# Kernel optimization log

Measured on AMD Instinct MI355X. Metric: run time of the kernel, lower is better.

## Reference

```python
import jax, jax.numpy as jnp
import numpy as np

ARITY = 2
DEPTH = 11          # full tree: levels 0..DEPTH, leaves at DEPTH
H = 1024
V = 32001           # vocab_size + 1 (null token)


def _preorder_perm(depth, arity):
    """Permutation mapping pre-order position -> BFS (level-concatenated) index."""
    offsets = np.concatenate([[0], np.cumsum(arity ** np.arange(depth + 1))])
    order = []
    def rec(d, p):
        order.append(int(offsets[d] + p))
        if d < depth:
            for c in range(arity):
                rec(d + 1, p * arity + c)
    rec(0, 0)
    return np.asarray(order, dtype=np.int32)

_PERM = _preorder_perm(DEPTH, ARITY)


def setup_inputs() -> dict:
    key = jax.random.key(0)
    ks = jax.random.split(key, 9)
    s = 0.02  # small init scale for numerical sanity
    return {
        "root_hidden": jax.random.normal(ks[0], (H,), jnp.float32),
        "W1v": jax.random.normal(ks[1], (H, 2 * H), jnp.float32) * s,
        "b1v": jax.random.normal(ks[2], (2 * H,), jnp.float32) * s,
        "W2v": jax.random.normal(ks[3], (2 * H, V), jnp.float32) * s,
        "b2v": jax.random.normal(ks[4], (V,), jnp.float32) * s,
        "W1c": jax.random.normal(ks[5], (H, 2 * H), jnp.float32) * s,
        "b1c": jax.random.normal(ks[6], (2 * H,), jnp.float32) * s,
        "W2c": jax.random.normal(ks[7], (2 * H, ARITY * H), jnp.float32) * s,
        "b2c": jax.random.normal(ks[8], (ARITY * H,), jnp.float32) * s,
    }


def _mlp(h, W1, b1, W2, b2):
    # Linear -> Sigmoid -> Linear (matches nn.Sequential in the torch module)
    return jax.nn.sigmoid(h @ W1 + b1) @ W2 + b2


def reference(root_hidden, W1v, b1v, W2v, b2v, W1c, b1c, W2c, b2c):
    # Level-wise vectorized sweep over the full tree (batches all nodes at a depth).
    h = root_hidden[None, :]                  # [1, H]
    prods = []
    for d in range(DEPTH + 1):
        prods.append(_mlp(h, W1v, b1v, W2v, b2v))     # [a^d, V]
        if d < DEPTH:
            # to_children then split into arity children per node
            h = _mlp(h, W1c, b1c, W2c, b2c).reshape(-1, H)  # [a^(d+1), H]
    raw = jnp.concatenate(prods, axis=0)      # BFS order, [N, V]
    raw = raw[_PERM]                          # reorder to pre-order (torch recursion order)
    return jax.nn.log_softmax(raw, axis=1)
```

## Files before the change

kernel.cpp:

```cpp
#include <hip/hip_runtime.h>
#include <hip/hip_bf16.h>

#define DEPTH_T 11
#define HDIM 1024
#define VDIM 32001
#define NNODES 4095
#define LDV 32008

typedef __attribute__((ext_vector_type(8))) short bf16x8;
typedef __attribute__((ext_vector_type(8))) unsigned short ushort8;
typedef __attribute__((ext_vector_type(4))) float floatx4;

__device__ __forceinline__ int preorder_pos(int m) {
    int q = m + 1;
    int d = 31 - __clz(q);
    int pos = 0;
    for (int i = 1; i <= d; ++i) {
        int b = (q >> (d - i)) & 1;
        pos += 1 + b * ((1 << (DEPTH_T - i + 1)) - 1);
    }
    return pos;
}

__device__ __forceinline__ float bf2f(unsigned short u) {
    return __uint_as_float(((unsigned)u) << 16);
}

#define BM 128
#define BN 128
#define BK 32

template<int MODE, bool SWAPG>
__global__ __launch_bounds__(256, 2) void gemm_bt(
    const __hip_bfloat16* __restrict__ A,
    const __hip_bfloat16* __restrict__ Bt,
    const float* __restrict__ bias,
    void* __restrict__ outp,
    int M, int N, int K, int ldout)
{
    __shared__ __align__(16) __hip_bfloat16 As[BM][BK];
    __shared__ __align__(16) __hip_bfloat16 Bs[BN][BK];

    const int tid  = threadIdx.x;
    const int wave = tid >> 6;
    const int lane = tid & 63;
    const int m0 = (SWAPG ? blockIdx.x : blockIdx.y) * BM;
    const int n0 = (SWAPG ? blockIdx.y : blockIdx.x) * BN;
    const int wm = (wave & 1) * 64;
    const int wn = (wave >> 1) * 64;

    floatx4 acc[4][4];
#pragma unroll
    for (int i = 0; i < 4; ++i)
#pragma unroll
        for (int j = 0; j < 4; ++j) acc[i][j] = (floatx4)0.0f;

    const int lrow = lane >> 2;
    const int lcol = (lane & 3) * 8;
    const int fr = lane & 15;
    const int fk = (lane >> 4) * 8;

    for (int k0 = 0; k0 < K; k0 += BK) {
        __syncthreads();
#pragma unroll
        for (int t = 0; t < 2; ++t) {
            const int r = (wave * 2 + t) * 16;
            int gm = m0 + r + lrow; gm = gm < M ? gm : M - 1;
            const __hip_bfloat16* gp = A + (size_t)gm * K + (k0 + lcol);
            __builtin_amdgcn_global_load_lds(
                (const __attribute__((address_space(1))) void*)gp,
                (__attribute__((address_space(3))) void*)(&As[r][0]),
                16, 0, 0);
        }
#pragma unroll
        for (int t = 0; t < 2; ++t) {
            const int r = (wave * 2 + t) * 16;
            int gn = n0 + r + lrow; gn = gn < N ? gn : N - 1;
            const __hip_bfloat16* gp = Bt + (size_t)gn * K + (k0 + lcol);
            __builtin_amdgcn_global_load_lds(
                (const __attribute__((address_space(1))) void*)gp,
                (__attribute__((address_space(3))) void*)(&Bs[r][0]),
                16, 0, 0);
        }
        __syncthreads();

        bf16x8 af[4], bfv[4];
#pragma unroll
        for (int i = 0; i < 4; ++i)
            af[i] = *(const bf16x8*)(&As[wm + i * 16 + fr][fk]);
#pragma unroll
        for (int j = 0; j < 4; ++j)
            bfv[j] = *(const bf16x8*)(&Bs[wn + j * 16 + fr][fk]);
#pragma unroll
        for (int i = 0; i < 4; ++i)
#pragma unroll
            for (int j = 0; j < 4; ++j)
                acc[i][j] = __builtin_amdgcn_mfma_f32_16x16x32_bf16(
                    af[i], bfv[j], acc[i][j], 0, 0, 0);
    }

    const int rq = (lane >> 4) * 4;
    if (MODE >= 2) {
#pragma unroll
        for (int i = 0; i < 4; ++i) {
#pragma unroll
            for (int r = 0; r < 4; ++r) {
                const int gm = m0 + wm + i * 16 + rq + r;
                if (gm >= M) continue;
                const size_t orow = (size_t)preorder_pos(gm) * ldout;
#pragma unroll
                for (int j = 0; j < 4; ++j) {
                    const int gn = n0 + wn + j * 16 + fr;
                    if (gn < N) {
                        float v = acc[i][j][r] + bias[gn];
                        if (MODE == 2) ((float*)outp)[orow + gn] = v;
                        else ((__hip_bfloat16*)outp)[orow + gn] = __float2bfloat16(v);
                    }
                }
            }
        }
    } else {
        __hip_bfloat16* O = (__hip_bfloat16*)outp;
#pragma unroll
        for (int i = 0; i < 4; ++i) {
#pragma unroll
            for (int r = 0; r < 4; ++r) {
                const int gm = m0 + wm + i * 16 + rq + r;
                if (gm >= M) continue;
#pragma unroll
                for (int j = 0; j < 4; ++j) {
                    const int gn = n0 + wn + j * 16 + fr;
                    if (gn < N) {
                        float v = acc[i][j][r] + bias[gn];
                        if (MODE == 0) v = 1.0f / (1.0f + __expf(-v));
                        O[(size_t)gm * ldout + gn] = __float2bfloat16(v);
                    }
                }
            }
        }
    }
}

#define B2M 256
#define B2N 256

template<int MODE>
__global__ __launch_bounds__(512, 2) void gemm256(
    const __hip_bfloat16* __restrict__ A,
    const __hip_bfloat16* __restrict__ Bt,
    const float* __restrict__ bias,
    void* __restrict__ outp,
    int M, int N, int K, int ldout)
{
    __shared__ __align__(16) char smem[131072];

    const int tid  = threadIdx.x;
    const int wave = tid >> 6;
    const int lane = tid & 63;
    const int m0 = blockIdx.x * B2M;
    const int n0 = blockIdx.y * B2N;
    const int wm = (wave >> 2) * 128;
    const int wn = (wave & 3) * 64;
    const int nkt = K >> 6;

    const int s_row = lane >> 3;
    const int s_col = ((lane & 7) ^ s_row) * 8;

    const int fr  = lane & 15;
    const int fkq = lane >> 4;
    const int swz = (fr & 7) << 4;
    const int c0  = (fkq * 16) ^ swz;
    const int c1  = (64 + fkq * 16) ^ swz;
    const int aoff = (wm + fr) * 128;
    const int boff = 32768 + (wn + fr) * 128;

    floatx4 acc[8][4];
#pragma unroll
    for (int i = 0; i < 8; ++i)
#pragma unroll
        for (int j = 0; j < 4; ++j) acc[i][j] = (floatx4)0.0f;

    bf16x8 a0[8], a1[8], b0[4], b1[4];

    auto stage = [&](int bsel, int mat, int h, int kt) {
        const int ktc = kt < nkt ? kt : 0;
        const __hip_bfloat16* gb = mat ? Bt : A;
        const int lim = mat ? N : M;
        const int g0  = mat ? n0 : m0;
#pragma unroll
        for (int inst = 0; inst < 2; ++inst) {
            const int rg = inst * 8 + wave;
            int gr = g0 + h * 128 + rg * 8 + s_row;
            gr = gr < lim ? gr : lim - 1;
            const __hip_bfloat16* gp = gb + (size_t)gr * K + (ktc * 64 + s_col);
            __builtin_amdgcn_global_load_lds(
                (const __attribute__((address_space(1))) void*)gp,
                (__attribute__((address_space(3))) void*)
                    (smem + bsel * 65536 + mat * 32768 + h * 16384 + rg * 1024),
                16, 0, 0);
        }
    };

#define RD_A(dst, bsel, cc) \
    _Pragma("unroll") \
    for (int i = 0; i < 8; ++i) \
        dst[i] = *(const bf16x8*)(smem + (bsel) * 65536 + aoff + i * 2048 + (cc));
#define RD_B(dst, bsel, cc) \
    _Pragma("unroll") \
    for (int j = 0; j < 4; ++j) \
        dst[j] = *(const bf16x8*)(smem + (bsel) * 65536 + boff + j * 2048 + (cc));
#define MM(ib, AA, BB) \
    _Pragma("unroll") \
    for (int i = 0; i < 4; ++i) \
    _Pragma("unroll") \
    for (int j = 0; j < 4; ++j) \
        acc[(ib) + i][j] = __builtin_amdgcn_mfma_f32_16x16x32_bf16( \
            AA[(ib) + i], BB[j], acc[(ib) + i][j], 0, 0, 0);
#define LGKM0  asm volatile("s_waitcnt lgkmcnt(0)" ::: "memory")
#define VM4    asm volatile("s_waitcnt vmcnt(4)" ::: "memory")
#define BAR    __builtin_amdgcn_s_barrier()
#define PRIO1  __builtin_amdgcn_s_setprio(1)
#define PRIO0  __builtin_amdgcn_s_setprio(0)

    stage(0, 0, 0, 0);
    stage(0, 0, 1, 0);
    stage(0, 1, 0, 0);
    stage(0, 1, 1, 0);
    stage(1, 0, 0, 1);
    stage(1, 0, 1, 1);
    VM4;
    BAR;

#pragma unroll 1
    for (int t = 0; t < nkt; t += 2) {
        RD_A(a0, 0, c0); RD_B(b0, 0, c0);
        stage(1, 1, 0, t + 1);
        BAR; LGKM0;
        PRIO1; MM(0, a0, b0); PRIO0;
        BAR;
        RD_A(a1, 0, c1); RD_B(b1, 0, c1);
        stage(1, 1, 1, t + 1);
        BAR; LGKM0;
        PRIO1; MM(4, a0, b0); PRIO0;
        BAR;
        stage(0, 0, 0, t + 2);
        BAR;
        PRIO1; MM(0, a1, b1); PRIO0;
        BAR;
        stage(0, 0, 1, t + 2);
        VM4;
        BAR;
        PRIO1; MM(4, a1, b1); PRIO0;
        BAR;
        RD_A(a0, 1, c0); RD_B(b0, 1, c0);
        stage(0, 1, 0, t + 2);
        BAR; LGKM0;
        PRIO1; MM(0, a0, b0); PRIO0;
        BAR;
        RD_A(a1, 1, c1); RD_B(b1, 1, c1);
        stage(0, 1, 1, t + 2);
        BAR; LGKM0;
        PRIO1; MM(4, a0, b0); PRIO0;
        BAR;
        stage(1, 0, 0, t + 3);
        BAR;
        PRIO1; MM(0, a1, b1); PRIO0;
        BAR;
        stage(1, 0, 1, t + 3);
        VM4;
        BAR;
        PRIO1; MM(4, a1, b1); PRIO0;
        BAR;
    }

#undef RD_A
#undef RD_B
#undef MM
#undef LGKM0
#undef VM4
#undef BAR
#undef PRIO1
#undef PRIO0

    const int rq = (lane >> 4) * 4;
    if (MODE >= 2) {
#pragma unroll
        for (int i = 0; i < 8; ++i) {
#pragma unroll
            for (int r = 0; r < 4; ++r) {
                const int gm = m0 + wm + i * 16 + rq + r;
                if (gm >= M) continue;
                const size_t orow = (size_t)preorder_pos(gm) * ldout;
#pragma unroll
                for (int j = 0; j < 4; ++j) {
                    const int gn = n0 + wn + j * 16 + fr;
                    if (gn < N) {
                        float v = acc[i][j][r] + bias[gn];
                        if (MODE == 2) ((float*)outp)[orow + gn] = v;
                        else ((__hip_bfloat16*)outp)[orow + gn] = __float2bfloat16(v);
                    }
                }
            }
        }
    } else {
        __hip_bfloat16* O = (__hip_bfloat16*)outp;
#pragma unroll
        for (int i = 0; i < 8; ++i) {
#pragma unroll
            for (int r = 0; r < 4; ++r) {
                const int gm = m0 + wm + i * 16 + rq + r;
                if (gm >= M) continue;
#pragma unroll
                for (int j = 0; j < 4; ++j) {
                    const int gn = n0 + wn + j * 16 + fr;
                    if (gn < N) {
                        float v = acc[i][j][r] + bias[gn];
                        if (MODE == 0) v = 1.0f / (1.0f + __expf(-v));
                        O[(size_t)gm * ldout + gn] = __float2bfloat16(v);
                    }
                }
            }
        }
    }
}

template<int MODE>
__global__ __launch_bounds__(256) void gemm_small(
    const __hip_bfloat16* __restrict__ A,
    const __hip_bfloat16* __restrict__ Bt,
    const float* __restrict__ bias,
    __hip_bfloat16* __restrict__ O,
    int M, int N, int K)
{
    const int wave = threadIdx.x >> 6, lane = threadIdx.x & 63;
    const int n0 = blockIdx.x * 64 + wave * 16;
    const int m0 = blockIdx.y * 16;
    const int fr = lane & 15, fk = (lane >> 4) * 8;

    int am = m0 + fr; am = am < M ? am : M - 1;
    const __hip_bfloat16* ap = A + (size_t)am * K + fk;
    const __hip_bfloat16* bp = Bt + (size_t)(n0 + fr) * K + fk;

    floatx4 acc = (floatx4)0.0f;
#pragma unroll 8
    for (int k0 = 0; k0 < K; k0 += 32) {
        bf16x8 av = *(const bf16x8*)(ap + k0);
        bf16x8 bv = *(const bf16x8*)(bp + k0);
        acc = __builtin_amdgcn_mfma_f32_16x16x32_bf16(av, bv, acc, 0, 0, 0);
    }

    const int rq = (lane >> 4) * 4;
    const int gn = n0 + fr;
    const float b = bias[gn];
#pragma unroll
    for (int r = 0; r < 4; ++r) {
        const int gm = m0 + rq + r;
        if (gm >= M) continue;
        float v = acc[r] + b;
        if (MODE == 0) v = 1.0f / (1.0f + __expf(-v));
        O[(size_t)gm * N + gn] = __float2bfloat16(v);
    }
}

__global__ __launch_bounds__(256) void transpose_to_bf16(
    const float* __restrict__ in, __hip_bfloat16* __restrict__ outT, int R, int C)
{
    __shared__ float tile[64][65];
    const int c0 = blockIdx.x * 64, r0 = blockIdx.y * 64;
    const int tx = threadIdx.x & 63, ty = threadIdx.x >> 6;
#pragma unroll
    for (int i = 0; i < 64; i += 4) {
        int r = r0 + ty + i, c = c0 + tx;
        tile[ty + i][tx] = (r < R && c < C) ? in[(size_t)r * C + c] : 0.0f;
    }
    __syncthreads();
#pragma unroll
    for (int i = 0; i < 64; i += 4) {
        int rr = c0 + ty + i, cc = r0 + tx;
        if (rr < C && cc < R) outT[(size_t)rr * R + cc] = __float2bfloat16(tile[tx][ty + i]);
    }
}

__global__ __launch_bounds__(256) void convert_root(
    const float* __restrict__ in, __hip_bfloat16* __restrict__ out)
{
    int i = blockIdx.x * 256 + threadIdx.x;
    if (i < HDIM) out[i] = __float2bfloat16(in[i]);
}

__global__ __launch_bounds__(256) void logsoftmax_bf16(
    const unsigned short* __restrict__ L, float* __restrict__ O)
{
    extern __shared__ char smem[];
    unsigned short* rb = (unsigned short*)smem;
    float* wred = (float*)(smem + 64016);
    const int tid = threadIdx.x, lane = tid & 63, wv = tid >> 6;
    const unsigned short* src = L + (size_t)blockIdx.x * LDV;

    float m = -3.0e38f;
    for (int j = tid * 8; j < 32000; j += 2048) {
        ushort8 u = *(const ushort8*)(src + j);
        *(ushort8*)(rb + j) = u;
#pragma unroll
        for (int t = 0; t < 8; ++t) m = fmaxf(m, bf2f(u[t]));
    }
    if (tid == 0) { unsigned short u = src[32000]; rb[32000] = u; m = fmaxf(m, bf2f(u)); }
#pragma unroll
    for (int off = 32; off; off >>= 1) m = fmaxf(m, __shfl_xor(m, off, 64));
    if (lane == 0) wred[wv] = m;
    __syncthreads();
    const float M4 = fmaxf(fmaxf(wred[0], wred[1]), fmaxf(wred[2], wred[3]));

    float s = 0.0f;
    for (int j = tid * 8; j < 32000; j += 2048) {
        ushort8 u = *(const ushort8*)(rb + j);
#pragma unroll
        for (int t = 0; t < 8; ++t) s += __expf(bf2f(u[t]) - M4);
    }
    if (tid == 0) s += __expf(bf2f(rb[32000]) - M4);
#pragma unroll
    for (int off = 32; off; off >>= 1) s += __shfl_xor(s, off, 64);
    if (lane == 0) wred[4 + wv] = s;
    __syncthreads();
    const float lse = M4 + __logf(wred[4] + wred[5] + wred[6] + wred[7]);

    float* dst = O + (size_t)blockIdx.x * VDIM;
    for (int j = tid * 8; j < 32000; j += 2048) {
        ushort8 u = *(const ushort8*)(rb + j);
#pragma unroll
        for (int t = 0; t < 8; ++t) dst[j + t] = bf2f(u[t]) - lse;
    }
    if (tid == 0) dst[32000] = bf2f(rb[32000]) - lse;
}

__global__ __launch_bounds__(256) void logsoftmax_rows(float* __restrict__ O, int n)
{
    __shared__ float sm[256], ssum[256];
    const int tid = threadIdx.x;
    float* p = O + (size_t)blockIdx.x * n;
    float m = -3.0e38f, s = 0.0f;
    for (int j = tid; j < n; j += 256) {
        float x = p[j];
        float nm = fmaxf(m, x);
        s = s * __expf(m - nm) + __expf(x - nm);
        m = nm;
    }
    sm[tid] = m; ssum[tid] = s;
    __syncthreads();
    for (int off = 128; off > 0; off >>= 1) {
        if (tid < off) {
            float m2 = sm[tid + off], s2 = ssum[tid + off];
            float nm = fmaxf(sm[tid], m2);
            ssum[tid] = ssum[tid] * __expf(sm[tid] - nm) + s2 * __expf(m2 - nm);
            sm[tid] = nm;
        }
        __syncthreads();
    }
    const float lse = sm[0] + __logf(ssum[0]);
    for (int j = tid; j < n; j += 256) p[j] -= lse;
}

extern "C" void kernel_launch(void* const* d_in, const int* in_sizes, int n_in,
                              void* d_out, int out_size, void* d_ws, size_t ws_size,
                              hipStream_t stream)
{
    const float* root = (const float*)d_in[0];
    const float* W1v  = (const float*)d_in[1];
    const float* b1v  = (const float*)d_in[2];
    const float* W2v  = (const float*)d_in[3];
    const float* b2v  = (const float*)d_in[4];
    const float* W1c  = (const float*)d_in[5];
    const float* b1c  = (const float*)d_in[6];
    const float* W2c  = (const float*)d_in[7];
    const float* b2c  = (const float*)d_in[8];

    char* ws = (char*)d_ws;
    __hip_bfloat16* Hall = (__hip_bfloat16*)(ws + 0);
    __hip_bfloat16* X1   = (__hip_bfloat16*)(ws +   8388608ull);
    __hip_bfloat16* Tt   = (__hip_bfloat16*)(ws +  25165824ull);
    __hip_bfloat16* W1vT = (__hip_bfloat16*)(ws +  29360128ull);
    __hip_bfloat16* W1cT = (__hip_bfloat16*)(ws +  33554432ull);
    __hip_bfloat16* W2cT = (__hip_bfloat16*)(ws +  37748736ull);
    __hip_bfloat16* W2vT = (__hip_bfloat16*)(ws +  46137344ull);
    __hip_bfloat16* Lb   = (__hip_bfloat16*)(ws + 177213440ull);
    const bool bf16_logits = ws_size >= 177213440ull + (size_t)NNODES * LDV * 2;

    dim3 blk(256);

    transpose_to_bf16<<<dim3( 32, 16), blk, 0, stream>>>(W1v, W1vT, 1024, 2048);
    transpose_to_bf16<<<dim3(501, 32), blk, 0, stream>>>(W2v, W2vT, 2048, VDIM);
    transpose_to_bf16<<<dim3( 32, 16), blk, 0, stream>>>(W1c, W1cT, 1024, 2048);
    transpose_to_bf16<<<dim3( 32, 32), blk, 0, stream>>>(W2c, W2cT, 2048, 2048);
    convert_root<<<dim3(4), blk, 0, stream>>>(root, Hall);

    for (int d = 0; d < DEPTH_T; ++d) {
        const int Md = 1 << d;
        __hip_bfloat16* Hd = Hall + (size_t)(Md - 1) * HDIM;
        __hip_bfloat16* Hn = Hall + (size_t)((2 << d) - 1) * HDIM;
        if (Md <= 256) {
            dim3 g(32, (Md + 15) / 16);
            gemm_small<0><<<g, blk, 0, stream>>>(Hd, W1cT, b1c, Tt, Md, 2048, 1024);
            gemm_small<1><<<g, blk, 0, stream>>>(Tt, W2cT, b2c, Hn, Md, 2048, 2048);
        } else {
            dim3 g(16, Md / 128);
            gemm_bt<0, false><<<g, blk, 0, stream>>>(Hd, W1cT, b1c, Tt, Md, 2048, 1024, 2048);
            gemm_bt<1, false><<<g, blk, 0, stream>>>(Tt, W2cT, b2c, Hn, Md, 2048, 2048, 2048);
        }
    }

    gemm_bt<0, false><<<dim3(16, 32), blk, 0, stream>>>(Hall, W1vT, b1v, X1, NNODES, 2048, 1024, 2048);
    if (bf16_logits) {
        gemm256<3><<<dim3(16, 126), dim3(512), 0, stream>>>(X1, W2vT, b2v, Lb, NNODES, VDIM, 2048, LDV);
        logsoftmax_bf16<<<dim3(NNODES), blk, 64048, stream>>>((const unsigned short*)Lb, (float*)d_out);
    } else {
        gemm_bt<2, true><<<dim3(32, 251), blk, 0, stream>>>(X1, W2vT, b2v, d_out, NNODES, VDIM, 2048, VDIM);
        logsoftmax_rows<<<dim3(NNODES), blk, 0, stream>>>((float*)d_out, VDIM);
    }
}
```

Baseline: 1.460 ms.

## Restructure 256x256 GEMM main loop into quadrant MFMA phases with XCD-aware block remap

The big vocab GEMM's k-loop is rewritten so LDS fragment reads are split into lo/hi halves of A and B. Each of four MFMA quadrant phases can then start after only partial lgkmcnt waits, with B tiles prefetched one stage earlier and sched_barriers pinning the order. The launch grid becomes 1D, and block ids are remapped so consecutive tiles land on the same XCD, aiming for better L2 reuse on the chiplet GPU. This adds more registers, finely tuned waitcnt counts and extra prologue loads, which risks correctness or stalls if the counts are wrong.

```diff
diff --git a/kernel.cpp b/kernel.cpp
--- a/kernel.cpp
+++ b/kernel.cpp
@@ -157,8 +157,15 @@
     const int tid  = threadIdx.x;
     const int wave = tid >> 6;
     const int lane = tid & 63;
-    const int m0 = blockIdx.x * B2M;
-    const int n0 = blockIdx.y * B2N;
+
+    const int nwx = (M + B2M - 1) / B2M;
+    const int nwy = (N + B2N - 1) / B2N;
+    const int nwg = nwx * nwy;
+    int wg = blockIdx.x;
+    if ((nwg & 7) == 0) wg = (wg & 7) * (nwg >> 3) + (wg >> 3);
+    const int m0 = (wg % nwx) * B2M;
+    const int n0 = (wg / nwx) * B2N;
+
     const int wm = (wave >> 2) * 128;
     const int wn = (wave & 3) * 64;
     const int nkt = K >> 6;
@@ -180,7 +187,7 @@
 #pragma unroll
         for (int j = 0; j < 4; ++j) acc[i][j] = (floatx4)0.0f;
 
-    bf16x8 a0[8], a1[8], b0[4], b1[4];
+    bf16x8 alo[8], ahi[8], blo[4], bhi[4];
 
     auto stage = [&](int bsel, int mat, int h, int kt) {
         const int ktc = kt < nkt ? kt : 0;
@@ -201,23 +208,39 @@
         }
     };
 
-#define RD_A(dst, bsel, cc) \
-    _Pragma("unroll") \
-    for (int i = 0; i < 8; ++i) \
-        dst[i] = *(const bf16x8*)(smem + (bsel) * 65536 + aoff + i * 2048 + (cc));
-#define RD_B(dst, bsel, cc) \
-    _Pragma("unroll") \
-    for (int j = 0; j < 4; ++j) \
-        dst[j] = *(const bf16x8*)(smem + (bsel) * 65536 + boff + j * 2048 + (cc));
-#define MM(ib, AA, BB) \
-    _Pragma("unroll") \
-    for (int i = 0; i < 4; ++i) \
-    _Pragma("unroll") \
-    for (int j = 0; j < 4; ++j) \
-        acc[(ib) + i][j] = __builtin_amdgcn_mfma_f32_16x16x32_bf16( \
-            AA[(ib) + i], BB[j], acc[(ib) + i][j], 0, 0, 0);
-#define LGKM0  asm volatile("s_waitcnt lgkmcnt(0)" ::: "memory")
-#define VM4    asm volatile("s_waitcnt vmcnt(4)" ::: "memory")
+#define RD_ALO(bsel) \
+    _Pragma("unroll") \
+    for (int f = 0; f < 4; ++f) { \
+        alo[f*2+0] = *(const bf16x8*)(smem + (bsel)*65536 + aoff + f*2048 + c0); \
+        alo[f*2+1] = *(const bf16x8*)(smem + (bsel)*65536 + aoff + f*2048 + c1); }
+#define RD_AHI(bsel) \
+    _Pragma("unroll") \
+    for (int f = 0; f < 4; ++f) { \
+        ahi[f*2+0] = *(const bf16x8*)(smem + (bsel)*65536 + aoff + (4+f)*2048 + c0); \
+        ahi[f*2+1] = *(const bf16x8*)(smem + (bsel)*65536 + aoff + (4+f)*2048 + c1); }
+#define RD_BLO(bsel) \
+    _Pragma("unroll") \
+    for (int j = 0; j < 2; ++j) { \
+        blo[j*2+0] = *(const bf16x8*)(smem + (bsel)*65536 + boff + j*2048 + c0); \
+        blo[j*2+1] = *(const bf16x8*)(smem + (bsel)*65536 + boff + j*2048 + c1); }
+#define RD_BHI(bsel) \
+    _Pragma("unroll") \
+    for (int j = 0; j < 2; ++j) { \
+        bhi[j*2+0] = *(const bf16x8*)(smem + (bsel)*65536 + boff + (2+j)*2048 + c0); \
+        bhi[j*2+1] = *(const bf16x8*)(smem + (bsel)*65536 + boff + (2+j)*2048 + c1); }
+#define MM_Q(IB, JB, AA, BB) \
+    _Pragma("unroll") \
+    for (int f = 0; f < 4; ++f) \
+    _Pragma("unroll") \
+    for (int jj = 0; jj < 2; ++jj) \
+    _Pragma("unroll") \
+    for (int ks = 0; ks < 2; ++ks) \
+        acc[(IB)+f][(JB)+jj] = __builtin_amdgcn_mfma_f32_16x16x32_bf16( \
+            AA[f*2+ks], BB[jj*2+ks], acc[(IB)+f][(JB)+jj], 0, 0, 0);
+
+#define VMC(n)  asm volatile("s_waitcnt vmcnt(" #n ")" ::: "memory")
+#define LGKM(n) asm volatile("s_waitcnt lgkmcnt(" #n ")" ::: "memory")
+#define SB0    __builtin_amdgcn_sched_barrier(0)
 #define BAR    __builtin_amdgcn_s_barrier()
 #define PRIO1  __builtin_amdgcn_s_setprio(1)
 #define PRIO0  __builtin_amdgcn_s_setprio(0)
@@ -228,56 +251,70 @@
     stage(0, 1, 1, 0);
     stage(1, 0, 0, 1);
     stage(1, 0, 1, 1);
-    VM4;
+    stage(1, 1, 0, 1);
+    stage(1, 1, 1, 1);
+    VMC(8);
     BAR;
+    RD_ALO(0); RD_BLO(0);
 
 #pragma unroll 1
     for (int t = 0; t < nkt; t += 2) {
-        RD_A(a0, 0, c0); RD_B(b0, 0, c0);
-        stage(1, 1, 0, t + 1);
-        BAR; LGKM0;
-        PRIO1; MM(0, a0, b0); PRIO0;
-        BAR;
-        RD_A(a1, 0, c1); RD_B(b1, 0, c1);
-        stage(1, 1, 1, t + 1);
-        BAR; LGKM0;
-        PRIO1; MM(4, a0, b0); PRIO0;
+        RD_AHI(0);
+        BAR;
+        LGKM(8); SB0;
+        PRIO1; MM_Q(0, 0, alo, blo); PRIO0;
+        BAR;
+        RD_BHI(0);
+        BAR;
+        LGKM(4); SB0;
+        PRIO1; MM_Q(4, 0, ahi, blo); PRIO0;
         BAR;
         stage(0, 0, 0, t + 2);
-        BAR;
-        PRIO1; MM(0, a1, b1); PRIO0;
-        BAR;
         stage(0, 0, 1, t + 2);
-        VM4;
-        BAR;
-        PRIO1; MM(4, a1, b1); PRIO0;
-        BAR;
-        RD_A(a0, 1, c0); RD_B(b0, 1, c0);
+        VMC(4); BAR;
+        LGKM(0); SB0;
+        PRIO1; MM_Q(0, 2, alo, bhi); PRIO0;
+        BAR;
+        RD_ALO(1); RD_BLO(1);
         stage(0, 1, 0, t + 2);
-        BAR; LGKM0;
-        PRIO1; MM(0, a0, b0); PRIO0;
-        BAR;
-        RD_A(a1, 1, c1); RD_B(b1, 1, c1);
         stage(0, 1, 1, t + 2);
-        BAR; LGKM0;
-        PRIO1; MM(4, a0, b0); PRIO0;
+        BAR;
+        LGKM(12); SB0;
+        PRIO1; MM_Q(4, 2, ahi, bhi); PRIO0;
+        BAR;
+        RD_AHI(1);
+        BAR;
+        LGKM(8); SB0;
+        PRIO1; MM_Q(0, 0, alo, blo); PRIO0;
+        BAR;
+        RD_BHI(1);
+        BAR;
+        LGKM(4); SB0;
+        PRIO1; MM_Q(4, 0, ahi, blo); PRIO0;
         BAR;
         stage(1, 0, 0, t + 3);
-        BAR;
-        PRIO1; MM(0, a1, b1); PRIO0;
-        BAR;
         stage(1, 0, 1, t + 3);
-        VM4;
-        BAR;
-        PRIO1; MM(4, a1, b1); PRIO0;
-        BAR;
-    }
-
-#undef RD_A
-#undef RD_B
-#undef MM
-#undef LGKM0
-#undef VM4
+        VMC(4); BAR;
+        LGKM(0); SB0;
+        PRIO1; MM_Q(0, 2, alo, bhi); PRIO0;
+        BAR;
+        RD_ALO(0); RD_BLO(0);
+        stage(1, 1, 0, t + 3);
+        stage(1, 1, 1, t + 3);
+        BAR;
+        LGKM(12); SB0;
+        PRIO1; MM_Q(4, 2, ahi, bhi); PRIO0;
+        BAR;
+    }
+
+#undef RD_ALO
+#undef RD_AHI
+#undef RD_BLO
+#undef RD_BHI
+#undef MM_Q
+#undef VMC
+#undef LGKM
+#undef SB0
 #undef BAR
 #undef PRIO1
 #undef PRIO0
@@ -510,7 +547,7 @@
 
     gemm_bt<0, false><<<dim3(16, 32), blk, 0, stream>>>(Hall, W1vT, b1v, X1, NNODES, 2048, 1024, 2048);
     if (bf16_logits) {
-        gemm256<3><<<dim3(16, 126), dim3(512), 0, stream>>>(X1, W2vT, b2v, Lb, NNODES, VDIM, 2048, LDV);
+        gemm256<3><<<dim3(16 * 126), dim3(512), 0, stream>>>(X1, W2vT, b2v, Lb, NNODES, VDIM, 2048, LDV);
         logsoftmax_bf16<<<dim3(NNODES), blk, 64048, stream>>>((const unsigned short*)Lb, (float*)d_out);
     } else {
         gemm_bt<2, true><<<dim3(32, 251), blk, 0, stream>>>(X1, W2vT, b2v, d_out, NNODES, VDIM, 2048, VDIM);
```

Result: no change. 1.478 ms (+1.2%).

## Fuse small tree levels into one cooperative kernel with grid syncs

Applied to the files above, without the earlier changes.

Replaces the 18 separate launches for tree levels 0-8 of the children MLP with one cooperative kernel. It loops over levels and uses grid.sync between the two GEMM stages and between levels. This cuts kernel launch overhead and inter-kernel gaps on the latency-bound small-M levels. In exchange it relies on cooperative launch with 256 blocks fitting co-resident, and it adds grid-wide barrier costs.

```diff
diff --git a/kernel.cpp b/kernel.cpp
--- a/kernel.cpp
+++ b/kernel.cpp
@@ -1,5 +1,8 @@
 #include <hip/hip_runtime.h>
 #include <hip/hip_bf16.h>
+#include <hip/hip_cooperative_groups.h>
+
+namespace cg = cooperative_groups;
 
 #define DEPTH_T 11
 #define HDIM 1024
@@ -362,6 +365,75 @@
     }
 }
 
+__global__ __launch_bounds__(256) void child_small_levels(
+    const __hip_bfloat16* __restrict__ W1cT, const float* __restrict__ b1c,
+    const __hip_bfloat16* __restrict__ W2cT, const float* __restrict__ b2c,
+    __hip_bfloat16* __restrict__ Hall, __hip_bfloat16* __restrict__ Tt)
+{
+    cg::grid_group grid = cg::this_grid();
+    const int wave = threadIdx.x >> 6, lane = threadIdx.x & 63;
+    const int gw = blockIdx.x * 4 + wave;
+    const int fr = lane & 15, fk = (lane >> 4) * 8;
+    const int rq = (lane >> 4) * 4;
+
+    for (int d = 0; d <= 8; ++d) {
+        const int Md = 1 << d;
+        const __hip_bfloat16* Hd = Hall + (size_t)(Md - 1) * HDIM;
+        __hip_bfloat16* Hn = Hall + (size_t)((2 << d) - 1) * HDIM;
+        const int mt = (Md + 15) >> 4;
+        const int ntiles = mt * 128;
+
+        for (int tile = gw; tile < ntiles; tile += 1024) {
+            const int m0 = (tile >> 7) * 16;
+            const int n0 = (tile & 127) * 16;
+            int am = m0 + fr; am = am < Md ? am : Md - 1;
+            const __hip_bfloat16* ap = Hd + (size_t)am * 1024 + fk;
+            const __hip_bfloat16* bp = W1cT + (size_t)(n0 + fr) * 1024 + fk;
+            floatx4 acc = (floatx4)0.0f;
+#pragma unroll 8
+            for (int k0 = 0; k0 < 1024; k0 += 32) {
+                bf16x8 av = *(const bf16x8*)(ap + k0);
+                bf16x8 bv = *(const bf16x8*)(bp + k0);
+                acc = __builtin_amdgcn_mfma_f32_16x16x32_bf16(av, bv, acc, 0, 0, 0);
+            }
+            const int gn = n0 + fr;
+            const float b = b1c[gn];
+#pragma unroll
+            for (int r = 0; r < 4; ++r) {
+                const int gm = m0 + rq + r;
+                if (gm >= Md) continue;
+                float v = 1.0f / (1.0f + __expf(-(acc[r] + b)));
+                Tt[(size_t)gm * 2048 + gn] = __float2bfloat16(v);
+            }
+        }
+        grid.sync();
+
+        for (int tile = gw; tile < ntiles; tile += 1024) {
+            const int m0 = (tile >> 7) * 16;
+            const int n0 = (tile & 127) * 16;
+            int am = m0 + fr; am = am < Md ? am : Md - 1;
+            const __hip_bfloat16* ap = Tt + (size_t)am * 2048 + fk;
+            const __hip_bfloat16* bp = W2cT + (size_t)(n0 + fr) * 2048 + fk;
+            floatx4 acc = (floatx4)0.0f;
+#pragma unroll 8
+            for (int k0 = 0; k0 < 2048; k0 += 32) {
+                bf16x8 av = *(const bf16x8*)(ap + k0);
+                bf16x8 bv = *(const bf16x8*)(bp + k0);
+                acc = __builtin_amdgcn_mfma_f32_16x16x32_bf16(av, bv, acc, 0, 0, 0);
+            }
+            const int gn = n0 + fr;
+            const float b = b2c[gn];
+#pragma unroll
+            for (int r = 0; r < 4; ++r) {
+                const int gm = m0 + rq + r;
+                if (gm >= Md) continue;
+                Hn[(size_t)gm * 2048 + gn] = __float2bfloat16(acc[r] + b);
+            }
+        }
+        grid.sync();
+    }
+}
+
 __global__ __launch_bounds__(256) void transpose_to_bf16(
     const float* __restrict__ in, __hip_bfloat16* __restrict__ outT, int R, int C)
 {
@@ -493,19 +565,19 @@
     transpose_to_bf16<<<dim3( 32, 32), blk, 0, stream>>>(W2c, W2cT, 2048, 2048);
     convert_root<<<dim3(4), blk, 0, stream>>>(root, Hall);
 
-    for (int d = 0; d < DEPTH_T; ++d) {
+    {
+        void* args[] = { (void*)&W1cT, (void*)&b1c, (void*)&W2cT, (void*)&b2c,
+                         (void*)&Hall, (void*)&Tt };
+        hipLaunchCooperativeKernel((const void*)child_small_levels,
+                                   dim3(256), dim3(256), args, 0, stream);
+    }
+    for (int d = 9; d < DEPTH_T; ++d) {
         const int Md = 1 << d;
         __hip_bfloat16* Hd = Hall + (size_t)(Md - 1) * HDIM;
         __hip_bfloat16* Hn = Hall + (size_t)((2 << d) - 1) * HDIM;
-        if (Md <= 256) {
-            dim3 g(32, (Md + 15) / 16);
-            gemm_small<0><<<g, blk, 0, stream>>>(Hd, W1cT, b1c, Tt, Md, 2048, 1024);
-            gemm_small<1><<<g, blk, 0, stream>>>(Tt, W2cT, b2c, Hn, Md, 2048, 2048);
-        } else {
-            dim3 g(16, Md / 128);
-            gemm_bt<0, false><<<g, blk, 0, stream>>>(Hd, W1cT, b1c, Tt, Md, 2048, 1024, 2048);
-            gemm_bt<1, false><<<g, blk, 0, stream>>>(Tt, W2cT, b2c, Hn, Md, 2048, 2048, 2048);
-        }
+        dim3 g(16, Md / 128);
+        gemm_bt<0, false><<<g, blk, 0, stream>>>(Hd, W1cT, b1c, Tt, Md, 2048, 1024, 2048);
+        gemm_bt<1, false><<<g, blk, 0, stream>>>(Tt, W2cT, b2c, Hn, Md, 2048, 2048, 2048);
     }
 
     gemm_bt<0, false><<<dim3(16, 32), blk, 0, stream>>>(Hall, W1vT, b1v, X1, NNODES, 2048, 1024, 2048);
```

New measurement: 1.865 ms. +27.7%, slower.

## Remap logits GEMM blocks per XCD for L2 reuse and precompute load pointers

Applied to the files above, without the earlier changes.

The logits GEMM launch becomes a 1D grid of 2048 blocks. Each block derives its M/N tile from blockIdx so that the blocks sent round-robin to each XCD share a compact group of M and N tiles, which should improve L2 reuse of the X1 and W2v operands. Blocks that map past the last N tile exit early. Per-thread global base pointers for the async LDS loads are now computed once before the loop, so the inner-loop address arithmetic is smaller. The risk is that the fixed mapping assumes the current grid shape and tile counts (16 M tiles, up to 128 N tiles).

```diff
diff --git a/kernel.cpp b/kernel.cpp
--- a/kernel.cpp
+++ b/kernel.cpp
@@ -157,8 +157,20 @@
     const int tid  = threadIdx.x;
     const int wave = tid >> 6;
     const int lane = tid & 63;
-    const int m0 = blockIdx.x * B2M;
-    const int n0 = blockIdx.y * B2N;
+
+    const int nwy = (N + B2N - 1) / B2N;
+    int mt, nt;
+    {
+        const int g = blockIdx.x >> 8;
+        const int i = blockIdx.x & 255;
+        const int k = i & 7, s = i >> 3;
+        mt = (k & 1) * 4 + (s & 3) + (g & 1) * 8;
+        nt = (k >> 1) * 8 + (s >> 2) + (g >> 1) * 32;
+    }
+    if (nt >= nwy) return;
+    const int m0 = mt * B2M;
+    const int n0 = nt * B2N;
+
     const int wm = (wave >> 2) * 128;
     const int wn = (wave & 3) * 64;
     const int nkt = K >> 6;
@@ -182,24 +194,31 @@
 
     bf16x8 a0[8], a1[8], b0[4], b1[4];
 
-    auto stage = [&](int bsel, int mat, int h, int kt) {
-        const int ktc = kt < nkt ? kt : 0;
-        const __hip_bfloat16* gb = mat ? Bt : A;
-        const int lim = mat ? N : M;
-        const int g0  = mat ? n0 : m0;
-#pragma unroll
-        for (int inst = 0; inst < 2; ++inst) {
-            const int rg = inst * 8 + wave;
-            int gr = g0 + h * 128 + rg * 8 + s_row;
-            gr = gr < lim ? gr : lim - 1;
-            const __hip_bfloat16* gp = gb + (size_t)gr * K + (ktc * 64 + s_col);
-            __builtin_amdgcn_global_load_lds(
-                (const __attribute__((address_space(1))) void*)gp,
-                (__attribute__((address_space(3))) void*)
-                    (smem + bsel * 65536 + mat * 32768 + h * 16384 + rg * 1024),
-                16, 0, 0);
-        }
+    auto mkb = [&](const __hip_bfloat16* gb, int g0, int lim, int h, int inst) {
+        int gr = g0 + h * 128 + (inst * 8 + wave) * 8 + s_row;
+        gr = gr < lim ? gr : lim - 1;
+        return gb + (size_t)gr * K + s_col;
     };
+    const __hip_bfloat16* pA00 = mkb(A,  m0, M, 0, 0);
+    const __hip_bfloat16* pA01 = mkb(A,  m0, M, 0, 1);
+    const __hip_bfloat16* pA10 = mkb(A,  m0, M, 1, 0);
+    const __hip_bfloat16* pA11 = mkb(A,  m0, M, 1, 1);
+    const __hip_bfloat16* pB00 = mkb(Bt, n0, N, 0, 0);
+    const __hip_bfloat16* pB01 = mkb(Bt, n0, N, 0, 1);
+    const __hip_bfloat16* pB10 = mkb(Bt, n0, N, 1, 0);
+    const __hip_bfloat16* pB11 = mkb(Bt, n0, N, 1, 1);
+
+#define STAGE(bsel, mat, h, PP0, PP1, kt) do { \
+    const int ko_ = ((kt) < nkt ? (kt) : 0) * 64; \
+    __builtin_amdgcn_global_load_lds( \
+        (const __attribute__((address_space(1))) void*)((PP0) + ko_), \
+        (__attribute__((address_space(3))) void*) \
+            (smem + (bsel)*65536 + (mat)*32768 + (h)*16384 + wave*1024), 16, 0, 0); \
+    __builtin_amdgcn_global_load_lds( \
+        (const __attribute__((address_space(1))) void*)((PP1) + ko_), \
+        (__attribute__((address_space(3))) void*) \
+            (smem + (bsel)*65536 + (mat)*32768 + (h)*16384 + 8192 + wave*1024), 16, 0, 0); \
+} while (0)
 
 #define RD_A(dst, bsel, cc) \
     _Pragma("unroll") \
@@ -222,57 +241,58 @@
 #define PRIO1  __builtin_amdgcn_s_setprio(1)
 #define PRIO0  __builtin_amdgcn_s_setprio(0)
 
-    stage(0, 0, 0, 0);
-    stage(0, 0, 1, 0);
-    stage(0, 1, 0, 0);
-    stage(0, 1, 1, 0);
-    stage(1, 0, 0, 1);
-    stage(1, 0, 1, 1);
+    STAGE(0, 0, 0, pA00, pA01, 0);
+    STAGE(0, 0, 1, pA10, pA11, 0);
+    STAGE(0, 1, 0, pB00, pB01, 0);
+    STAGE(0, 1, 1, pB10, pB11, 0);
+    STAGE(1, 0, 0, pA00, pA01, 1);
+    STAGE(1, 0, 1, pA10, pA11, 1);
     VM4;
     BAR;
 
 #pragma unroll 1
     for (int t = 0; t < nkt; t += 2) {
         RD_A(a0, 0, c0); RD_B(b0, 0, c0);
-        stage(1, 1, 0, t + 1);
+        STAGE(1, 1, 0, pB00, pB01, t + 1);
         BAR; LGKM0;
         PRIO1; MM(0, a0, b0); PRIO0;
         BAR;
         RD_A(a1, 0, c1); RD_B(b1, 0, c1);
-        stage(1, 1, 1, t + 1);
+        STAGE(1, 1, 1, pB10, pB11, t + 1);
         BAR; LGKM0;
         PRIO1; MM(4, a0, b0); PRIO0;
         BAR;
-        stage(0, 0, 0, t + 2);
+        STAGE(0, 0, 0, pA00, pA01, t + 2);
         BAR;
         PRIO1; MM(0, a1, b1); PRIO0;
         BAR;
-        stage(0, 0, 1, t + 2);
+        STAGE(0, 0, 1, pA10, pA11, t + 2);
         VM4;
         BAR;
         PRIO1; MM(4, a1, b1); PRIO0;
         BAR;
         RD_A(a0, 1, c0); RD_B(b0, 1, c0);
-        stage(0, 1, 0, t + 2);
+        STAGE(0, 1, 0, pB00, pB01, t + 2);
         BAR; LGKM0;
         PRIO1; MM(0, a0, b0); PRIO0;
         BAR;
         RD_A(a1, 1, c1); RD_B(b1, 1, c1);
-        stage(0, 1, 1, t + 2);
+        STAGE(0, 1, 1, pB10, pB11, t + 2);
         BAR; LGKM0;
         PRIO1; MM(4, a0, b0); PRIO0;
         BAR;
-        stage(1, 0, 0, t + 3);
+        STAGE(1, 0, 0, pA00, pA01, t + 3);
         BAR;
         PRIO1; MM(0, a1, b1); PRIO0;
         BAR;
-        stage(1, 0, 1, t + 3);
+        STAGE(1, 0, 1, pA10, pA11, t + 3);
         VM4;
         BAR;
         PRIO1; MM(4, a1, b1); PRIO0;
         BAR;
     }
 
+#undef STAGE
 #undef RD_A
 #undef RD_B
 #undef MM
@@ -510,7 +530,7 @@
 
     gemm_bt<0, false><<<dim3(16, 32), blk, 0, stream>>>(Hall, W1vT, b1v, X1, NNODES, 2048, 1024, 2048);
     if (bf16_logits) {
-        gemm256<3><<<dim3(16, 126), dim3(512), 0, stream>>>(X1, W2vT, b2v, Lb, NNODES, VDIM, 2048, LDV);
+        gemm256<3><<<dim3(2048), dim3(512), 0, stream>>>(X1, W2vT, b2v, Lb, NNODES, VDIM, 2048, LDV);
         logsoftmax_bf16<<<dim3(NNODES), blk, 64048, stream>>>((const unsigned short*)Lb, (float*)d_out);
     } else {
         gemm_bt<2, true><<<dim3(32, 251), blk, 0, stream>>>(X1, W2vT, b2v, d_out, NNODES, VDIM, 2048, VDIM);
```

New measurement: 1.440 ms. No clear change (-1.3%).
